# Kernel tuning notes

Hardware: AMD Instinct MI355X
Metric: run time of the kernel (lower is better)

Reference implementation:

```python
import jax, jax.numpy as jnp
import numpy as np

B, S, H = 8, 2048, 2048

def setup_inputs() -> dict:
    key = jax.random.key(0)
    ks = jax.random.split(key, 7)
    return {
        "time_decay": jax.random.normal(ks[0], (H,), dtype=jnp.float32),
        "key": jax.random.normal(ks[1], (B, S, H), dtype=jnp.float32),
        "time_first": jax.random.normal(ks[2], (H,), dtype=jnp.float32),
        "value": jax.random.normal(ks[3], (B, S, H), dtype=jnp.float32),
        "max_state": jax.random.normal(ks[4], (B, H), dtype=jnp.float32),
        "num_state": jax.random.normal(ks[5], (B, H), dtype=jnp.float32),
        "den_state": jax.random.uniform(ks[6], (B, H), dtype=jnp.float32),
    }

def _wkv(time_decay, k, time_first, v, max_state, num_state, den_state):
    f32 = jnp.float32
    td = -jnp.exp(time_decay.astype(f32))          # [H]
    tf = time_first.astype(f32)                    # [H]
    k = k.astype(f32)
    v = v.astype(f32)

    def step(carry, kv_t):
        m, num, den = carry                        # each [B,H]
        kt, vt = kv_t                              # each [B,H]
        # output branch: include time_first bonus
        mo = jnp.maximum(m, kt + tf)
        e1o = jnp.exp(m - mo)
        e2o = jnp.exp(kt + tf - mo)
        out = (e1o * num + e2o * vt) / (e1o * den + e2o)
        # state branch: apply decay
        ms = jnp.maximum(m + td, kt)
        e1s = jnp.exp(m + td - ms)
        e2s = jnp.exp(kt - ms)
        return (ms, e1s * num + e2s * vt, e1s * den + e2s), out

    carry0 = (max_state.astype(f32), num_state.astype(f32), den_state.astype(f32))
    # scan over time: move seq axis to front -> [S,B,H]
    (m, num, den), outs = jax.lax.scan(
        step, carry0, (jnp.swapaxes(k, 0, 1), jnp.swapaxes(v, 0, 1)))
    output = jnp.swapaxes(outs, 0, 1)              # [B,S,H]
    return output, m, num, den

def reference(time_decay, key, time_first, value, max_state, num_state, den_state):
    return _wkv(time_decay, key, time_first, value, max_state, num_state, den_state)
```

## Files before the change

### kernel.cpp

```cpp
#include <hip/hip_runtime.h>


#define TILE 128
#define NW   16
#define SUB  (TILE / NW)

#define VMW0  asm volatile("s_waitcnt vmcnt(0)" ::: "memory")
#define VMW8  asm volatile("s_waitcnt vmcnt(8)" ::: "memory")
#define BARR  asm volatile("s_waitcnt lgkmcnt(0)\n\ts_barrier" ::: "memory")

__device__ __forceinline__ float ex2(float x)  { return __builtin_amdgcn_exp2f(x); }
__device__ __forceinline__ float rcpf(float x) { return __builtin_amdgcn_rcpf(x); }

__device__ __forceinline__ void dma16(const float* g, float* l) {
    __builtin_amdgcn_global_load_lds(
        (const __attribute__((address_space(1))) unsigned int*)g,
        (__attribute__((address_space(3))) unsigned int*)l, 16, 0, 0);
}

__global__ __launch_bounds__(1024)
void wkv_fwd(const float* __restrict__ td_in, const float* __restrict__ kin,
             const float* __restrict__ tf_in, const float* __restrict__ vin,
             const float* __restrict__ m0, const float* __restrict__ n0,
             const float* __restrict__ d0,
             float* __restrict__ out, float* __restrict__ m_out,
             float* __restrict__ n_out, float* __restrict__ dn_out,
             int B, int S, int H)
{
    __shared__ float kbuf[2][TILE][64];
    __shared__ float vbuf[2][TILE][64];
    __shared__ float smry[2][NW][3][64];
    __shared__ float cry[2][3][64];

    const int tid  = threadIdx.x;
    const int lane = tid & 63;
    const int w    = tid >> 6;

    const int bpb = H >> 6;
    const int b   = blockIdx.x / bpb;
    const int hb  = (blockIdx.x - b * bpb) << 6;
    const int h   = hb + lane;
    const int g   = b * H + h;

    constexpr float Cc = 1.4426950408889634f;
    constexpr float IC = 0.6931471805599453f;

    const float tds  = -ex2(td_in[h] * Cc) * Cc;
    const float tfs  = tf_in[h] * Cc;
    const float dseg = tds * (float)SUB;

    if (w == 0) {
        cry[0][0][lane] = m0[g] * Cc;
        cry[0][1][lane] = n0[g];
        cry[0][2][lane] = d0[g];
    }

    const size_t base = (size_t)b * (size_t)S * (size_t)H + (size_t)hb;
    const float* gk = kin + base;
    const float* gv = vin + base;
    float*       go = out + base;

    const int sub = lane >> 4;
    const int c4  = (lane & 15) << 2;

    const int ntiles = S / TILE;

    #pragma unroll
    for (int i = 0; i < SUB / 4; ++i) {
        const int r = w * SUB + i * 4;
        dma16(gk + (size_t)(r + sub) * H + c4, &kbuf[0][r][0]);
        dma16(gv + (size_t)(r + sub) * H + c4, &vbuf[0][r][0]);
    }

    float fM = 0.f, fN = 0.f, fD = 0.f;

    for (int it = 0; it < ntiles; ++it) {
        const int p = it & 1;
        if (it == 0) { VMW0; } else { VMW8; }

        if (it + 1 < ntiles) {
            const int np = p ^ 1;
            const size_t t1 = (size_t)(it + 1) * TILE;
            #pragma unroll
            for (int i = 0; i < SUB / 4; ++i) {
                const int r = w * SUB + i * 4;
                dma16(gk + (t1 + r + sub) * (size_t)H + c4, &kbuf[np][r][0]);
                dma16(gv + (t1 + r + sub) * (size_t)H + c4, &vbuf[np][r][0]);
            }
        }

        float kt[SUB], vt[SUB];
        float plm[SUB - 1], pln[SUB - 1], pld[SUB - 1];
        float lm = -1e30f, ln = 0.f, ld = 0.f;
        #pragma unroll
        for (int j = 0; j < SUB; ++j) {
            kt[j] = kbuf[p][w * SUB + j][lane] * Cc;
            vt[j] = vbuf[p][w * SUB + j][lane];
            const float mpd = lm + tds;
            const float d   = mpd - kt[j];
            const float e   = ex2(-fabsf(d));
            const bool  c   = d >= 0.f;
            const float e1  = c ? 1.f : e;
            const float e2  = c ? e : 1.f;
            ln  = e1 * ln  + e2 * vt[j];
            ld  = e1 * ld  + e2;
            lm  = fmaxf(mpd, kt[j]);
            if (j < SUB - 1) { plm[j] = lm; pln[j] = ln; pld[j] = ld; }
        }
        smry[p][w][0][lane] = lm;
        smry[p][w][1][lane] = ln;
        smry[p][w][2][lane] = ld;
        BARR;

        float M = cry[p][0][lane];
        float N = cry[p][1][lane];
        float D = cry[p][2][lane];
        for (int j = 0; j < w; ++j) {
            const float Md = M + dseg;
            const float sm = smry[p][j][0][lane];
            const float d  = Md - sm;
            const float e  = ex2(-fabsf(d));
            const bool  c  = d >= 0.f;
            const float a  = c ? 1.f : e;
            const float bb = c ? e : 1.f;
            N = a * N + bb * smry[p][j][1][lane];
            D = a * D + bb * smry[p][j][2][lane];
            M = fmaxf(Md, sm);
        }

        if (w == NW - 1) {
            const float Md = M + dseg;
            const float d  = Md - lm;
            const float e  = ex2(-fabsf(d));
            const bool  c  = d >= 0.f;
            const float a  = c ? 1.f : e;
            const float bb = c ? e : 1.f;
            fN = a * N + bb * ln;
            fD = a * D + bb * ld;
            fM = fmaxf(Md, lm);
            cry[p ^ 1][0][lane] = fM;
            cry[p ^ 1][1][lane] = fN;
            cry[p ^ 1][2][lane] = fD;
        }

        float* po = go + ((size_t)it * TILE + (size_t)w * SUB) * (size_t)H;
        {
            const float ktf = kt[0] + tfs;
            const float dd  = M - ktf;
            const float eo  = ex2(-fabsf(dd));
            const bool  co  = dd >= 0.f;
            const float e1o = co ? 1.f : eo;
            const float e2o = co ? eo : 1.f;
            po[lane] = (e1o * N + e2o * vt[0]) * rcpf(fmaf(e1o, D, e2o));
        }
        float Md = M;
        #pragma unroll
        for (int j = 1; j < SUB; ++j) {
            Md += tds;
            const float sm = plm[j - 1];
            const float dl = Md - sm;
            const float e  = ex2(-fabsf(dl));
            const bool  c  = dl >= 0.f;
            const float a  = c ? 1.f : e;
            const float bb = c ? e : 1.f;
            const float Nc = a * N + bb * pln[j - 1];
            const float Dc = a * D + bb * pld[j - 1];
            const float Mc = fmaxf(Md, sm);
            const float ktf = kt[j] + tfs;
            const float dd  = Mc - ktf;
            const float eo  = ex2(-fabsf(dd));
            const bool  co  = dd >= 0.f;
            const float e1o = co ? 1.f : eo;
            const float e2o = co ? eo : 1.f;
            po[(size_t)j * H + lane] =
                (e1o * Nc + e2o * vt[j]) * rcpf(fmaf(e1o, Dc, e2o));
        }
    }

    if (w == NW - 1) {
        m_out[g]  = fM * IC;
        n_out[g]  = fN;
        dn_out[g] = fD;
    }
}

__global__ __launch_bounds__(64)
void wkv_fwd_serial(const float* __restrict__ td_in, const float* __restrict__ kin,
                    const float* __restrict__ tf_in, const float* __restrict__ vin,
                    const float* __restrict__ m0, const float* __restrict__ n0,
                    const float* __restrict__ d0,
                    float* __restrict__ out, float* __restrict__ m_out,
                    float* __restrict__ n_out, float* __restrict__ dn_out,
                    int B, int S, int H)
{
    const int g = blockIdx.x * 64 + threadIdx.x;
    if (g >= B * H) return;
    const int b = g / H;
    const int h = g - b * H;
    constexpr float Cc = 1.4426950408889634f, IC = 0.6931471805599453f;
    const float tds = -ex2(td_in[h] * Cc) * Cc;
    const float tfs = tf_in[h] * Cc;
    float M = m0[g] * Cc, N = n0[g], D = d0[g];
    const size_t base = (size_t)b * S * H + h;
    for (int t = 0; t < S; ++t) {
        const float kt  = kin[base + (size_t)t * H] * Cc;
        const float vt  = vin[base + (size_t)t * H];
        const float ktf = kt + tfs;
        const float mo  = fmaxf(M, ktf);
        const float e1o = ex2(M - mo), e2o = ex2(ktf - mo);
        out[base + (size_t)t * H] = (e1o * N + e2o * vt) * rcpf(e1o * D + e2o);
        const float mpd = M + tds;
        const float ms  = fmaxf(mpd, kt);
        const float e1s = ex2(mpd - ms), e2s = ex2(kt - ms);
        N = e1s * N + e2s * vt;
        D = e1s * D + e2s;
        M = ms;
    }
    m_out[g] = M * IC; n_out[g] = N; dn_out[g] = D;
}

extern "C" void kernel_launch(void* const* d_in, const int* in_sizes, int n_in,
                              void* d_out, int out_size, void* d_ws, size_t ws_size,
                              hipStream_t stream)
{
    const float* time_decay = (const float*)d_in[0];
    const float* key        = (const float*)d_in[1];
    const float* time_first = (const float*)d_in[2];
    const float* value      = (const float*)d_in[3];
    const float* max_state  = (const float*)d_in[4];
    const float* num_state  = (const float*)d_in[5];
    const float* den_state  = (const float*)d_in[6];

    const int H  = in_sizes[0];
    const int BH = in_sizes[4];
    const int B  = BH / H;
    const int S  = in_sizes[1] / BH;

    float* out    = (float*)d_out;
    float* m_out  = out + (size_t)B * (size_t)S * (size_t)H;
    float* n_out  = m_out + BH;
    float* dn_out = n_out + BH;

    if ((H % 64 == 0) && (S % TILE == 0)) {
        const int grid = BH / 64;
        wkv_fwd<<<grid, 1024, 0, stream>>>(time_decay, key, time_first, value,
                                           max_state, num_state, den_state,
                                           out, m_out, n_out, dn_out, B, S, H);
    } else {
        const int grid = (BH + 63) / 64;
        wkv_fwd_serial<<<grid, 64, 0, stream>>>(time_decay, key, time_first, value,
                                                max_state, num_state, den_state,
                                                out, m_out, n_out, dn_out, B, S, H);
    }
}
```

Before: 338.8 us.

## Prefetch k/v tiles into registers instead of LDS DMA double buffering

Replaces the global-to-LDS DMA double buffer with direct per-lane register loads of the next tile's k and v, ping-ponging between two register arrays through a lambda unrolled twice. This drops the LDS round trip and the explicit vmcnt waits. The cross-wave prefix loop is also fully unrolled with a predicate so the smry loads can be issued early. In exchange it raises register pressure in a 1024-thread block, and each lane now does 4-byte loads instead of 16-byte DMA transactions.

```diff
diff --git a/kernel.cpp b/kernel.cpp
--- a/kernel.cpp
+++ b/kernel.cpp
@@ -5,18 +5,10 @@
 #define NW   16
 #define SUB  (TILE / NW)
 
-#define VMW0  asm volatile("s_waitcnt vmcnt(0)" ::: "memory")
-#define VMW8  asm volatile("s_waitcnt vmcnt(8)" ::: "memory")
 #define BARR  asm volatile("s_waitcnt lgkmcnt(0)\n\ts_barrier" ::: "memory")
 
 __device__ __forceinline__ float ex2(float x)  { return __builtin_amdgcn_exp2f(x); }
 __device__ __forceinline__ float rcpf(float x) { return __builtin_amdgcn_rcpf(x); }
-
-__device__ __forceinline__ void dma16(const float* g, float* l) {
-    __builtin_amdgcn_global_load_lds(
-        (const __attribute__((address_space(1))) unsigned int*)g,
-        (__attribute__((address_space(3))) unsigned int*)l, 16, 0, 0);
-}
 
 __global__ __launch_bounds__(1024)
 void wkv_fwd(const float* __restrict__ td_in, const float* __restrict__ kin,
@@ -27,8 +19,6 @@
              float* __restrict__ n_out, float* __restrict__ dn_out,
              int B, int S, int H)
 {
-    __shared__ float kbuf[2][TILE][64];
-    __shared__ float vbuf[2][TILE][64];
     __shared__ float smry[2][NW][3][64];
     __shared__ float cry[2][3][64];
 
@@ -60,42 +50,42 @@
     const float* gv = vin + base;
     float*       go = out + base;
 
-    const int sub = lane >> 4;
-    const int c4  = (lane & 15) << 2;
-
     const int ntiles = S / TILE;
 
-    #pragma unroll
-    for (int i = 0; i < SUB / 4; ++i) {
-        const int r = w * SUB + i * 4;
-        dma16(gk + (size_t)(r + sub) * H + c4, &kbuf[0][r][0]);
-        dma16(gv + (size_t)(r + sub) * H + c4, &vbuf[0][r][0]);
-    }
-
     float fM = 0.f, fN = 0.f, fD = 0.f;
 
-    for (int it = 0; it < ntiles; ++it) {
+    float ka[SUB], va[SUB], kb[SUB], vb[SUB];
+
+    {
+        const size_t t0 = (size_t)w * SUB;
+        #pragma unroll
+        for (int j = 0; j < SUB; ++j) {
+            ka[j] = gk[(t0 + j) * (size_t)H + lane];
+            va[j] = gv[(t0 + j) * (size_t)H + lane];
+        }
+    }
+
+    auto body = [&](int it, float (&ck)[SUB], float (&cv)[SUB],
+                    float (&nk)[SUB], float (&nv)[SUB])
+                __attribute__((always_inline)) -> void {
+        if (it + 1 < ntiles) {
+            const size_t t1 = (size_t)(it + 1) * TILE + (size_t)w * SUB;
+            #pragma unroll
+            for (int j = 0; j < SUB; ++j) {
+                nk[j] = gk[(t1 + j) * (size_t)H + lane];
+                nv[j] = gv[(t1 + j) * (size_t)H + lane];
+            }
+        }
+
         const int p = it & 1;
-        if (it == 0) { VMW0; } else { VMW8; }
-
-        if (it + 1 < ntiles) {
-            const int np = p ^ 1;
-            const size_t t1 = (size_t)(it + 1) * TILE;
-            #pragma unroll
-            for (int i = 0; i < SUB / 4; ++i) {
-                const int r = w * SUB + i * 4;
-                dma16(gk + (t1 + r + sub) * (size_t)H + c4, &kbuf[np][r][0]);
-                dma16(gv + (t1 + r + sub) * (size_t)H + c4, &vbuf[np][r][0]);
-            }
-        }
 
         float kt[SUB], vt[SUB];
         float plm[SUB - 1], pln[SUB - 1], pld[SUB - 1];
         float lm = -1e30f, ln = 0.f, ld = 0.f;
         #pragma unroll
         for (int j = 0; j < SUB; ++j) {
-            kt[j] = kbuf[p][w * SUB + j][lane] * Cc;
-            vt[j] = vbuf[p][w * SUB + j][lane];
+            kt[j] = ck[j] * Cc;
+            vt[j] = cv[j];
             const float mpd = lm + tds;
             const float d   = mpd - kt[j];
             const float e   = ex2(-fabsf(d));
@@ -115,17 +105,22 @@
         float M = cry[p][0][lane];
         float N = cry[p][1][lane];
         float D = cry[p][2][lane];
-        for (int j = 0; j < w; ++j) {
-            const float Md = M + dseg;
+        #pragma unroll
+        for (int j = 0; j < NW - 1; ++j) {
             const float sm = smry[p][j][0][lane];
-            const float d  = Md - sm;
-            const float e  = ex2(-fabsf(d));
-            const bool  c  = d >= 0.f;
-            const float a  = c ? 1.f : e;
-            const float bb = c ? e : 1.f;
-            N = a * N + bb * smry[p][j][1][lane];
-            D = a * D + bb * smry[p][j][2][lane];
-            M = fmaxf(Md, sm);
+            const float sn = smry[p][j][1][lane];
+            const float sd = smry[p][j][2][lane];
+            if (j < w) {
+                const float Md = M + dseg;
+                const float d  = Md - sm;
+                const float e  = ex2(-fabsf(d));
+                const bool  c  = d >= 0.f;
+                const float a  = c ? 1.f : e;
+                const float bb = c ? e : 1.f;
+                N = a * N + bb * sn;
+                D = a * D + bb * sd;
+                M = fmaxf(Md, sm);
+            }
         }
 
         if (w == NW - 1) {
@@ -175,7 +170,14 @@
             po[(size_t)j * H + lane] =
                 (e1o * Nc + e2o * vt[j]) * rcpf(fmaf(e1o, Dc, e2o));
         }
-    }
+    };
+
+    int it = 0;
+    for (; it + 1 < ntiles; it += 2) {
+        body(it,     ka, va, kb, vb);
+        body(it + 1, kb, vb, ka, va);
+    }
+    if (it < ntiles) body(it, ka, va, kb, vb);
 
     if (w == NW - 1) {
         m_out[g]  = fM * IC;
```

New measurement: 337.0 us. About the same (-0.5%).
